# Kernel optimization log

Measured on AMD Instinct MI355X. Metric: run time of the kernel, lower is better.

Reference implementation:

```python
import jax, jax.numpy as jnp
import numpy as np

DIM = 512
HEADS = 16
DIM_HEAD = 64
INNER = HEADS * DIM_HEAD
MAX_T = 32
BASE = 10000.0


def rotate_half(t):
    t1, t2 = jnp.split(t, 2, axis=-1)
    return jnp.concatenate((-t2, t1), axis=-1)


def setup_inputs() -> dict:
    key = jax.random.key(0)
    ks = jax.random.split(key, 12)
    B, T, S = 2, 16, 128
    x = jax.random.normal(ks[0], (B, T, S, DIM), dtype=jnp.float32)
    y = jax.random.normal(ks[1], (B, T, S, DIM), dtype=jnp.float32)
    temporal_mask = jax.random.randint(ks[2], (B, T, T), 0, 2).astype(jnp.int32)
    sc = 1.0 / np.sqrt(DIM)
    Wq = jax.random.normal(ks[3], (DIM, INNER), dtype=jnp.float32) * sc
    Wk = jax.random.normal(ks[4], (DIM, INNER), dtype=jnp.float32) * sc
    Wv = jax.random.normal(ks[5], (DIM, INNER), dtype=jnp.float32) * sc
    Wo = jax.random.normal(ks[6], (INNER, DIM), dtype=jnp.float32) / np.sqrt(INNER)
    bo = jnp.zeros((DIM,), dtype=jnp.float32)
    pos_emb = jax.random.normal(ks[7], (MAX_T, DIM), dtype=jnp.float32)
    gate_w = jax.random.normal(ks[8], (DIM, 1), dtype=jnp.float32) * sc
    gate_b = jnp.zeros((1,), dtype=jnp.float32)
    return {"x": x, "y": y, "temporal_mask": temporal_mask, "Wq": Wq, "Wk": Wk,
            "Wv": Wv, "Wo": Wo, "bo": bo, "pos_emb": pos_emb,
            "gate_w": gate_w, "gate_b": gate_b}


def reference(x, y, temporal_mask, Wq, Wk, Wv, Wo, bo, pos_emb, gate_w, gate_b):
    B, T, S, D = x.shape
    n = T * S
    scale = DIM_HEAD ** (-0.5)
    # temporal positional embedding (T <= MAX_T path)
    tp = pos_emb[:T][None, :, None, :]  # [1,T,1,D]
    x = x + tp
    y = y + tp
    xf = x.reshape(B, n, D)
    yf = y.reshape(B, n, D)
    # NOTE: k is computed from x (as in the source), v from y
    q = (xf @ Wq).reshape(B, n, HEADS, DIM_HEAD).transpose(0, 2, 1, 3)
    k = (xf @ Wk).reshape(B, n, HEADS, DIM_HEAD).transpose(0, 2, 1, 3)
    v = (yf @ Wv).reshape(B, n, HEADS, DIM_HEAD).transpose(0, 2, 1, 3)
    # RoPE over flattened token index
    inv_freq = 1.0 / (BASE ** (jnp.arange(0, DIM_HEAD, 2, dtype=jnp.float32) / DIM_HEAD))
    freqs = jnp.arange(n, dtype=jnp.float32)[:, None] * inv_freq[None, :]  # [n, d/2]
    emb = jnp.concatenate((freqs, freqs), axis=-1)  # [n, d]
    fc = jnp.cos(emb)[None, None, :, :]
    fs = jnp.sin(emb)[None, None, :, :]
    q = q * fc + rotate_half(q) * fs
    k = k * fc + rotate_half(k) * fs
    dots = jnp.einsum('bhid,bhjd->bhij', q, k) * scale  # [B,H,n,n]
    # expand temporal mask [B,T,T] -> [B,1,n,n] block structure
    m = jnp.repeat(jnp.repeat(temporal_mask, S, axis=1), S, axis=2)[:, None, :, :]
    dots = jnp.where(m == 0, -jnp.inf, dots)
    attn = jax.nn.softmax(dots, axis=-1)
    out = jnp.einsum('bhij,bhjd->bhid', attn, v)  # [B,H,n,d]
    out = out.transpose(0, 2, 1, 3).reshape(B, n, INNER)
    out = out @ Wo + bo
    out = out.reshape(B, T, S, D)
    gate = jax.nn.sigmoid(out @ gate_w + gate_b)  # [B,T,S,1]
    return out * gate
```

## Files before the change

### kernel.cpp

```cpp
#include <hip/hip_runtime.h>
#include <hip/hip_bf16.h>

typedef __attribute__((ext_vector_type(4))) short short4v;
typedef __attribute__((ext_vector_type(8))) short short8v;
typedef __attribute__((ext_vector_type(4))) float float4v;
typedef __attribute__((ext_vector_type(2))) unsigned int uint2v;
typedef __attribute__((ext_vector_type(4))) unsigned int uint4v;

#define NTOK 2048
#define MROWS 4096
#define DMODEL 512
#define NINNER 1024
#define DH 64
#define HH 16
#define LOG2E 1.4426950408889634f

__device__ __forceinline__ unsigned short b2s(float f) {
    __hip_bfloat16 h = __float2bfloat16(f);
    return __builtin_bit_cast(unsigned short, h);
}
__device__ __forceinline__ float bf2f(unsigned short h) {
    unsigned int u = ((unsigned int)h) << 16;
    return __builtin_bit_cast(float, u);
}

__device__ __forceinline__ float4v mfma32(short8v a, short8v b, float4v c) {
    return __builtin_amdgcn_mfma_f32_16x16x32_bf16(a, b, c, 0, 0, 0);
}

__device__ __forceinline__ void gld16(const void* g, void* l) {
    __builtin_amdgcn_global_load_lds((const __attribute__((address_space(1))) void*)g,
                                     (__attribute__((address_space(3))) void*)l, 16, 0, 0);
}

__global__ void k_pre(const float* __restrict__ x, const float* __restrict__ y,
                      const float* __restrict__ pe,
                      unsigned short* __restrict__ xpb, unsigned short* __restrict__ ypb,
                      const float* __restrict__ Wq, const float* __restrict__ Wk,
                      const float* __restrict__ Wv, const float* __restrict__ Wo,
                      const float* __restrict__ gwv, const float* __restrict__ gbv,
                      const float* __restrict__ bo,
                      unsigned short* __restrict__ wall, unsigned short* __restrict__ wot,
                      float* __restrict__ ctab, float* __restrict__ stab,
                      unsigned short* __restrict__ gvp, float* __restrict__ bgp) {
    __shared__ float tl[64][65];
    const int blk = blockIdx.x;
    const int tid = threadIdx.x;
    if (blk < 2048) {
        int e0 = (blk * 256 + tid) * 4;
        int row = e0 >> 9, col = e0 & 511;
        int t = (row & (NTOK - 1)) >> 7;
        const float4v xv = *(const float4v*)(x + e0);
        const float4v yv = *(const float4v*)(y + e0);
        const float4v pv = *(const float4v*)(pe + t * DMODEL + col);
        short4v xo, yo;
#pragma unroll
        for (int i = 0; i < 4; ++i) {
            xo[i] = (short)b2s(xv[i] + pv[i]);
            yo[i] = (short)b2s(yv[i] + pv[i]);
        }
        *(short4v*)(xpb + e0) = xo;
        *(short4v*)(ypb + e0) = yo;
    } else if (blk < 2560) {
        int t = blk - 2048;
        const float* W;
        unsigned short* dst;
        int K, N, k0, n0;
        if (t < 384) {
            int which = t / 128, tile = t % 128;
            W = (which == 0) ? Wq : (which == 1) ? Wk : Wv;
            dst = wall + (size_t)which * 1024 * 512;
            K = 512; N = 1024;
            k0 = (tile >> 4) * 64; n0 = (tile & 15) * 64;
        } else {
            int tile = t - 384;
            W = Wo; dst = wot;
            K = 1024; N = 512;
            k0 = (tile >> 3) * 64; n0 = (tile & 7) * 64;
        }
        int tx = tid & 63, ty4 = tid >> 6;
#pragma unroll
        for (int p = 0; p < 16; ++p) {
            int ky = p * 4 + ty4;
            tl[ky][tx] = W[(size_t)(k0 + ky) * N + n0 + tx];
        }
        __syncthreads();
#pragma unroll
        for (int p = 0; p < 16; ++p) {
            int ny = p * 4 + ty4;
            dst[(size_t)(n0 + ny) * K + k0 + tx] = b2s(tl[tx][ny]);
        }
    } else if (blk < 2816) {
        int idx = (blk - 2560) * 256 + tid;
        int p = idx >> 5, j = idx & 31;
        float invf = powf(10000.0f, -(float)(2 * j) * (1.0f / 64.0f));
        float f = (float)p * invf;
        ctab[idx] = cosf(f);
        stab[idx] = sinf(f);
    } else if (blk < 2832) {
        int base = (blk - 2816) * 64;
        int w = tid >> 6, l = tid & 63, l16 = l & 15, g = l >> 4;
        int row = base + w * 16 + l16;
        const float* wr = Wo + (size_t)row * 512 + g * 128;
        const float* gr = gwv + g * 128;
        float s = 0.f;
#pragma unroll
        for (int t = 0; t < 32; ++t) {
            float4v a = *(const float4v*)(wr + t * 4);
            float4v b = *(const float4v*)(gr + t * 4);
            s += a[0] * b[0] + a[1] * b[1] + a[2] * b[2] + a[3] * b[3];
        }
        s += __shfl_xor(s, 16);
        s += __shfl_xor(s, 32);
        if (g == 0) gvp[row] = b2s(s);
    } else {
        if (tid < 64) {
            float s = 0.f;
#pragma unroll
            for (int t = 0; t < 8; ++t) s += bo[tid + t * 64] * gwv[tid + t * 64];
#pragma unroll
            for (int off = 32; off > 0; off >>= 1) s += __shfl_xor(s, off);
            if (tid == 0) bgp[0] = s + gbv[0];
        }
    }
}

__global__ __launch_bounds__(256) void k_qkv(const unsigned short* __restrict__ A,
                                             const unsigned short* __restrict__ A2,
                                             const unsigned short* __restrict__ Bt,
                                             unsigned short* __restrict__ Cq,
                                             unsigned short* __restrict__ Ck,
                                             unsigned short* __restrict__ Cvv,
                                             const float* __restrict__ ctab,
                                             const float* __restrict__ stab,
                                             float scale) {
    __shared__ unsigned short Ab[2][4096];
    __shared__ unsigned short Bb[2][4096];
    const int tid = threadIdx.x;
    const int w = tid >> 6, l = tid & 63, l16 = l & 15, g = l >> 4;
    const int wm = w >> 1, wn = w & 1;
    const int m0 = blockIdx.y * 128, n0 = blockIdx.x * 128;
    const unsigned short* Ap = (n0 >= 2048) ? A2 : A;
    float4v acc[4][4];
#pragma unroll
    for (int i = 0; i < 4; ++i)
#pragma unroll
        for (int j = 0; j < 4; ++j) acc[i][j] = (float4v){0.f, 0.f, 0.f, 0.f};

    auto stage = [&](int t, int buf) {
        int k0 = t * 32;
#pragma unroll
        for (int it = 0; it < 2; ++it) {
            int f = it * 4 + w;
            gld16(Ap + (size_t)(m0 + f * 16 + l16) * 512 + k0 + g * 8, &Ab[buf][f * 512]);
            gld16(Bt + (size_t)(n0 + f * 16 + l16) * 512 + k0 + g * 8, &Bb[buf][f * 512]);
        }
    };

    stage(0, 0);
    __syncthreads();
    for (int t = 0; t < 16; ++t) {
        const int cur = t & 1;
        if (t + 1 < 16) stage(t + 1, cur ^ 1);
        short8v af[4], bf[4];
#pragma unroll
        for (int mi = 0; mi < 4; ++mi)
            af[mi] = *(const short8v*)&Ab[cur][(wm * 4 + mi) * 512 + l * 8];
#pragma unroll
        for (int nj = 0; nj < 4; ++nj)
            bf[nj] = *(const short8v*)&Bb[cur][(wn * 4 + nj) * 512 + l * 8];
        __builtin_amdgcn_s_setprio(1);
#pragma unroll
        for (int mi = 0; mi < 4; ++mi)
#pragma unroll
            for (int nj = 0; nj < 4; ++nj)
                acc[mi][nj] = mfma32(af[mi], bf[nj], acc[mi][nj]);
        __builtin_amdgcn_s_setprio(0);
        __syncthreads();
    }

    const int hh = (n0 + wn * 64) >> 6;
    const int head = hh & 15;
    if (hh < 32) {
        unsigned short* out = (hh < 16) ? Cq : Ck;
        const float sc = (hh < 16) ? scale : 1.0f;
#pragma unroll
        for (int mi = 0; mi < 4; ++mi)
#pragma unroll
            for (int r = 0; r < 4; ++r) {
                int row = m0 + wm * 64 + mi * 16 + g * 4 + r;
                int b = row >> 11, pos = row & (NTOK - 1);
                const float* cr = ctab + pos * 32;
                const float* sr = stab + pos * 32;
                unsigned short* ob = out + (size_t)((b * HH + head) * NTOK + pos) * DH;
#pragma unroll
                for (int nj = 0; nj < 2; ++nj) {
                    int j = nj * 16 + l16;
                    float c = cr[j], s = sr[j];
                    float v1 = acc[mi][nj][r], v2 = acc[mi][nj + 2][r];
                    ob[j] = b2s((v1 * c - v2 * s) * sc);
                    ob[j + 32] = b2s((v2 * c + v1 * s) * sc);
                }
            }
    } else {
#pragma unroll
        for (int mi = 0; mi < 4; ++mi)
#pragma unroll
            for (int nj = 0; nj < 4; ++nj) {
                int d = nj * 16 + l16;
                int row0 = m0 + wm * 64 + mi * 16 + g * 4;
                int b = row0 >> 11, pos0 = row0 & (NTOK - 1);
                short4v o;
#pragma unroll
                for (int r = 0; r < 4; ++r) o[r] = (short)b2s(acc[mi][nj][r]);
                *(short4v*)(Cvv + (size_t)((b * HH + head) * DH + d) * NTOK + pos0) = o;
            }
    }
}

__global__ __launch_bounds__(256) void k_oproj(const unsigned short* __restrict__ A,
                                               const unsigned short* __restrict__ Bt,
                                               const float* __restrict__ bo,
                                               const unsigned short* __restrict__ gv,
                                               const float* __restrict__ bgp,
                                               float* __restrict__ out) {
    __shared__ unsigned short Ab[2][2048];
    __shared__ unsigned short Bb[2][2048];
    const int tid = threadIdx.x;
    const int w = tid >> 6, l = tid & 63, l16 = l & 15, g = l >> 4;
    const int m0 = blockIdx.y * 64, n0 = blockIdx.x * 64;
    float4v acc[4];
#pragma unroll
    for (int j = 0; j < 4; ++j) acc[j] = (float4v){0.f, 0.f, 0.f, 0.f};
    float4v gacc = (float4v){0.f, 0.f, 0.f, 0.f};

    auto stage = [&](int t, int buf) {
        int k0 = t * 32;
        gld16(A + (size_t)(m0 + w * 16 + l16) * 1024 + k0 + g * 8, &Ab[buf][w * 512]);
        gld16(Bt + (size_t)(n0 + w * 16 + l16) * 1024 + k0 + g * 8, &Bb[buf][w * 512]);
    };

    stage(0, 0);
    __syncthreads();
    for (int t = 0; t < 32; ++t) {
        const int cur = t & 1;
        if (t + 1 < 32) stage(t + 1, cur ^ 1);
        short8v af = *(const short8v*)&Ab[cur][w * 512 + l * 8];
        short8v bf[4];
#pragma unroll
        for (int nj = 0; nj < 4; ++nj)
            bf[nj] = *(const short8v*)&Bb[cur][nj * 512 + l * 8];
        short8v gvf = *(const short8v*)(gv + t * 32 + g * 8);
        __builtin_amdgcn_s_setprio(1);
#pragma unroll
        for (int nj = 0; nj < 4; ++nj)
            acc[nj] = mfma32(af, bf[nj], acc[nj]);
        gacc = mfma32(af, gvf, gacc);
        __builtin_amdgcn_s_setprio(0);
        __syncthreads();
    }
    const float bg = bgp[0];
    float gl[4];
#pragma unroll
    for (int r = 0; r < 4; ++r) gl[r] = 1.0f / (1.0f + __expf(-(gacc[r] + bg)));
#pragma unroll
    for (int nj = 0; nj < 4; ++nj) {
        int col = n0 + nj * 16 + l16;
        float bv = bo[col];
#pragma unroll
        for (int r = 0; r < 4; ++r) {
            int row = m0 + w * 16 + g * 4 + r;
            out[(size_t)row * 512 + col] = (acc[nj][r] + bv) * gl[r];
        }
    }
}

__global__ __launch_bounds__(512) void k_attn(const unsigned short* __restrict__ qh,
                                              const unsigned short* __restrict__ kh,
                                              const unsigned short* __restrict__ vt,
                                              const int* __restrict__ tmask,
                                              unsigned short* __restrict__ otmp) {
    __shared__ unsigned short Kb[3][4096];
    __shared__ unsigned short Vb[2][4096];
    __shared__ int tlist[33];
    const int blk = blockIdx.x;
    const int u = (blk & 7) * 64 + (blk >> 3);
    const int ti = u & 15, h = (u >> 4) & 15, b = u >> 8;
    const int tid = threadIdx.x, w = tid >> 6, l = tid & 63, l16 = l & 15, g = l >> 4;
    if (tid == 0) {
        int c = 0;
        for (int j = 0; j < 16; ++j)
            if (tmask[(b * 16 + ti) * 16 + j]) { tlist[c++] = 2 * j; tlist[c++] = 2 * j + 1; }
        tlist[32] = c;
    }
    __syncthreads();
    const int cnt = tlist[32];
    const unsigned short* qb = qh + (size_t)((b * HH + h) * NTOK) * DH;
    const unsigned short* kb = kh + (size_t)((b * HH + h) * NTOK) * DH;
    const unsigned short* vb = vt + (size_t)((b * HH + h) * DH) * NTOK;
    const int q0 = ti * 128 + w * 16;

    short8v qf[2];
#pragma unroll
    for (int c = 0; c < 2; ++c)
        qf[c] = *(const short8v*)(qb + (size_t)(q0 + l16) * DH + c * 32 + g * 8);

    short8v ones;
#pragma unroll
    for (int j = 0; j < 8; ++j) ones[j] = (short)0x3F80;

    float4v oacc[4];
#pragma unroll
    for (int i = 0; i < 4; ++i) oacc[i] = (float4v){0.f, 0.f, 0.f, 0.f};
    float4v lsum = (float4v){0.f, 0.f, 0.f, 0.f};
    float mx = -1e30f;
    uint4v vrg;
    float4v sA[4], sB[4];

    auto stageK = [&](int st, int buf) {
        const unsigned short* ga =
            kb + (size_t)(st * 64 + (w >> 1) * 16 + l16) * DH + (w & 1) * 32 + g * 8;
        gld16(ga, &Kb[buf][w * 512]);
    };
    auto loadV = [&](int st) {
        const unsigned short* ga =
            vb + (size_t)((w >> 1) * 16 + l16) * NTOK + st * 64 + (w & 1) * 32 + g * 4;
        uint2v lo = *(const uint2v*)ga;
        uint2v hi = *(const uint2v*)(ga + 16);
        vrg = (uint4v){lo[0], lo[1], hi[0], hi[1]};
    };
    auto writeV = [&](int buf) {
        *(uint4v*)&Vb[buf][w * 512 + l * 8] = vrg;
    };
    auto qkcomp = [&](int buf, float4v (&s)[4]) {
#pragma unroll
        for (int jk = 0; jk < 4; ++jk) s[jk] = (float4v){0.f, 0.f, 0.f, 0.f};
        __builtin_amdgcn_s_setprio(1);
#pragma unroll
        for (int jk = 0; jk < 4; ++jk) {
            short8v kf0 = *(const short8v*)&Kb[buf][(jk * 2 + 0) * 512 + l * 8];
            short8v kf1 = *(const short8v*)&Kb[buf][(jk * 2 + 1) * 512 + l * 8];
            s[jk] = mfma32(kf0, qf[0], s[jk]);
            s[jk] = mfma32(kf1, qf[1], s[jk]);
        }
        __builtin_amdgcn_s_setprio(0);
    };

    auto body = [&](int i, float4v (&scur)[4], float4v (&snext)[4]) {
        const bool pre1 = (i + 1 < cnt), pre2 = (i + 2 < cnt);
        if (pre2) stageK(tlist[i + 2], (i + 2) % 3);
        if (pre1) loadV(tlist[i + 1]);
        float tm = -1e30f;
#pragma unroll
        for (int jk = 0; jk < 4; ++jk) {
            float4v s4 = scur[jk];
            tm = fmaxf(tm, fmaxf(fmaxf(s4[0], s4[1]), fmaxf(s4[2], s4[3])));
        }
        tm = fmaxf(tm, __shfl_xor(tm, 16));
        tm = fmaxf(tm, __shfl_xor(tm, 32));
        if (!__all(tm <= mx + 8.0f)) {
            float mnew = fmaxf(mx, tm);
            float alpha = exp2f(mx - mnew);
#pragma unroll
            for (int r = 0; r < 4; ++r) lsum[r] *= alpha;
#pragma unroll
            for (int md = 0; md < 4; ++md)
#pragma unroll
                for (int r = 0; r < 4; ++r) oacc[md][r] *= alpha;
            mx = mnew;
        }
        if (pre1) qkcomp((i + 1) % 3, snext);
        short8v pf[2];
#pragma unroll
        for (int cc = 0; cc < 2; ++cc) {
            short8v pv;
#pragma unroll
            for (int r = 0; r < 4; ++r) {
                pv[r] = (short)b2s(exp2f(scur[2 * cc][r] - mx));
                pv[r + 4] = (short)b2s(exp2f(scur[2 * cc + 1][r] - mx));
            }
            pf[cc] = pv;
        }
        __builtin_amdgcn_s_setprio(1);
#pragma unroll
        for (int cc = 0; cc < 2; ++cc) lsum = mfma32(ones, pf[cc], lsum);
#pragma unroll
        for (int md = 0; md < 4; ++md)
#pragma unroll
            for (int cc = 0; cc < 2; ++cc) {
                short8v vf = *(const short8v*)&Vb[i & 1][(md * 2 + cc) * 512 + l * 8];
                oacc[md] = mfma32(vf, pf[cc], oacc[md]);
            }
        __builtin_amdgcn_s_setprio(0);
        if (pre1) writeV((i + 1) & 1);
        __syncthreads();
    };

    if (cnt > 0) {
        stageK(tlist[0], 0);
        loadV(tlist[0]);
        if (cnt > 1) stageK(tlist[1], 1);
        writeV(0);
        __syncthreads();
        qkcomp(0, sA);
        for (int i = 0; i < cnt; i += 2) {
            body(i, sA, sB);
            if (i + 1 < cnt) body(i + 1, sB, sA);
        }
    }
    float lrow = lsum[0];
    float inv = lrow > 0.f ? 1.0f / lrow : 0.f;
    int q = q0 + l16;
#pragma unroll
    for (int md = 0; md < 4; ++md) {
        short4v o;
#pragma unroll
        for (int r = 0; r < 4; ++r) o[r] = (short)b2s(oacc[md][r] * inv);
        *(short4v*)(otmp + (size_t)(b * NTOK + q) * NINNER + h * DH + md * 16 + g * 4) = o;
    }
}

extern "C" void kernel_launch(void* const* d_in, const int* in_sizes, int n_in,
                              void* d_out, int out_size, void* d_ws, size_t ws_size,
                              hipStream_t stream) {
    (void)in_sizes; (void)n_in; (void)out_size; (void)ws_size;
    const float* x = (const float*)d_in[0];
    const float* y = (const float*)d_in[1];
    const int* tmask = (const int*)d_in[2];
    const float* Wq = (const float*)d_in[3];
    const float* Wk = (const float*)d_in[4];
    const float* Wv = (const float*)d_in[5];
    const float* Wo = (const float*)d_in[6];
    const float* bo = (const float*)d_in[7];
    const float* pe = (const float*)d_in[8];
    const float* gw = (const float*)d_in[9];
    const float* gb = (const float*)d_in[10];

    char* ws = (char*)d_ws;
    const size_t MB = 1u << 20;
    unsigned short* xpb  = (unsigned short*)(ws + 0);
    unsigned short* ypb  = (unsigned short*)(ws + 4 * MB);
    unsigned short* wall = (unsigned short*)(ws + 8 * MB);
    unsigned short* wot  = (unsigned short*)(ws + 11 * MB);
    unsigned short* qh   = (unsigned short*)(ws + 12 * MB);
    unsigned short* kh   = (unsigned short*)(ws + 20 * MB);
    unsigned short* vt   = (unsigned short*)(ws + 28 * MB);
    unsigned short* otm  = (unsigned short*)(ws + 36 * MB);
    float* ct = (float*)(ws + 44 * MB);
    float* st = (float*)(ws + 44 * MB + 256 * 1024);
    unsigned short* gv = (unsigned short*)(ws + 45 * MB);
    float* bg = (float*)(ws + 45 * MB + 4096);
    float* outp = (float*)d_out;

    k_pre<<<2833, 256, 0, stream>>>(x, y, pe, xpb, ypb, Wq, Wk, Wv, Wo, gw, gb, bo,
                                    wall, wot, ct, st, gv, bg);
    k_qkv<<<dim3(24, 32), 256, 0, stream>>>(xpb, ypb, wall, qh, kh, vt, ct, st,
                                            0.125f * LOG2E);
    k_attn<<<512, 512, 0, stream>>>(qh, kh, vt, tmask, otm);
    k_oproj<<<dim3(8, 64), 256, 0, stream>>>(otm, wot, bo, gv, bg, outp);
}
```

Before: 115.6 us.

## Process two key tiles per iteration with four-deep K/V LDS ring buffers

Restructures the attention inner loop to handle two 64-key tiles per iteration. Both QK products, a shared max/rescale and both PV products run together, and K and V for the next pair are prefetched into a four-slot LDS ring. This halves the number of block-wide barriers and online-softmax rescale checks and gives more independent MFMA work to schedule. In exchange it uses more LDS (four K and four V buffers) and more registers, which may lower occupancy. It also removes the previous overlap of the next tile's QK with the current tile's softmax.

```diff
diff --git a/kernel.cpp b/kernel.cpp
--- a/kernel.cpp
+++ b/kernel.cpp
@@ -280,8 +280,8 @@
                                               const unsigned short* __restrict__ vt,
                                               const int* __restrict__ tmask,
                                               unsigned short* __restrict__ otmp) {
-    __shared__ unsigned short Kb[3][4096];
-    __shared__ unsigned short Vb[2][4096];
+    __shared__ unsigned short Kb[4][4096];
+    __shared__ unsigned short Vb[4][4096];
     __shared__ int tlist[33];
     const int blk = blockIdx.x;
     const int u = (blk & 7) * 64 + (blk >> 3);
@@ -314,7 +314,7 @@
     for (int i = 0; i < 4; ++i) oacc[i] = (float4v){0.f, 0.f, 0.f, 0.f};
     float4v lsum = (float4v){0.f, 0.f, 0.f, 0.f};
     float mx = -1e30f;
-    uint4v vrg;
+    uint4v vrgA, vrgB;
     float4v sA[4], sB[4];
 
     auto stageK = [&](int st, int buf) {
@@ -322,15 +322,15 @@
             kb + (size_t)(st * 64 + (w >> 1) * 16 + l16) * DH + (w & 1) * 32 + g * 8;
         gld16(ga, &Kb[buf][w * 512]);
     };
-    auto loadV = [&](int st) {
+    auto loadV = [&](int st, uint4v& vr) {
         const unsigned short* ga =
             vb + (size_t)((w >> 1) * 16 + l16) * NTOK + st * 64 + (w & 1) * 32 + g * 4;
         uint2v lo = *(const uint2v*)ga;
         uint2v hi = *(const uint2v*)(ga + 16);
-        vrg = (uint4v){lo[0], lo[1], hi[0], hi[1]};
-    };
-    auto writeV = [&](int buf) {
-        *(uint4v*)&Vb[buf][w * 512 + l * 8] = vrg;
+        vr = (uint4v){lo[0], lo[1], hi[0], hi[1]};
+    };
+    auto writeV = [&](int buf, const uint4v& vr) {
+        *(uint4v*)&Vb[buf][w * 512 + l * 8] = vr;
     };
     auto qkcomp = [&](int buf, float4v (&s)[4]) {
 #pragma unroll
@@ -345,19 +345,30 @@
         }
         __builtin_amdgcn_s_setprio(0);
     };
-
-    auto body = [&](int i, float4v (&scur)[4], float4v (&snext)[4]) {
-        const bool pre1 = (i + 1 < cnt), pre2 = (i + 2 < cnt);
-        if (pre2) stageK(tlist[i + 2], (i + 2) % 3);
-        if (pre1) loadV(tlist[i + 1]);
-        float tm = -1e30f;
-#pragma unroll
-        for (int jk = 0; jk < 4; ++jk) {
-            float4v s4 = scur[jk];
-            tm = fmaxf(tm, fmaxf(fmaxf(s4[0], s4[1]), fmaxf(s4[2], s4[3])));
-        }
-        tm = fmaxf(tm, __shfl_xor(tm, 16));
-        tm = fmaxf(tm, __shfl_xor(tm, 32));
+    auto packexp = [&](const float4v (&s)[4], short8v (&pf)[2]) {
+#pragma unroll
+        for (int cc = 0; cc < 2; ++cc) {
+            short8v pv;
+#pragma unroll
+            for (int r = 0; r < 4; ++r) {
+                pv[r] = (short)b2s(exp2f(s[2 * cc][r] - mx));
+                pv[r + 4] = (short)b2s(exp2f(s[2 * cc + 1][r] - mx));
+            }
+            pf[cc] = pv;
+        }
+    };
+    auto pvcomp = [&](int buf, const short8v (&pf)[2]) {
+#pragma unroll
+        for (int cc = 0; cc < 2; ++cc) lsum = mfma32(ones, pf[cc], lsum);
+#pragma unroll
+        for (int md = 0; md < 4; ++md)
+#pragma unroll
+            for (int cc = 0; cc < 2; ++cc) {
+                short8v vf = *(const short8v*)&Vb[buf][(md * 2 + cc) * 512 + l * 8];
+                oacc[md] = mfma32(vf, pf[cc], oacc[md]);
+            }
+    };
+    auto rescale = [&](float tm) {
         if (!__all(tm <= mx + 8.0f)) {
             float mnew = fmaxf(mx, tm);
             float alpha = exp2f(mx - mnew);
@@ -369,43 +380,58 @@
                 for (int r = 0; r < 4; ++r) oacc[md][r] *= alpha;
             mx = mnew;
         }
-        if (pre1) qkcomp((i + 1) % 3, snext);
-        short8v pf[2];
-#pragma unroll
-        for (int cc = 0; cc < 2; ++cc) {
-            short8v pv;
-#pragma unroll
-            for (int r = 0; r < 4; ++r) {
-                pv[r] = (short)b2s(exp2f(scur[2 * cc][r] - mx));
-                pv[r + 4] = (short)b2s(exp2f(scur[2 * cc + 1][r] - mx));
-            }
-            pf[cc] = pv;
-        }
-        __builtin_amdgcn_s_setprio(1);
-#pragma unroll
-        for (int cc = 0; cc < 2; ++cc) lsum = mfma32(ones, pf[cc], lsum);
-#pragma unroll
-        for (int md = 0; md < 4; ++md)
-#pragma unroll
-            for (int cc = 0; cc < 2; ++cc) {
-                short8v vf = *(const short8v*)&Vb[i & 1][(md * 2 + cc) * 512 + l * 8];
-                oacc[md] = mfma32(vf, pf[cc], oacc[md]);
-            }
-        __builtin_amdgcn_s_setprio(0);
-        if (pre1) writeV((i + 1) & 1);
-        __syncthreads();
     };
 
     if (cnt > 0) {
         stageK(tlist[0], 0);
-        loadV(tlist[0]);
-        if (cnt > 1) stageK(tlist[1], 1);
-        writeV(0);
+        loadV(tlist[0], vrgA);
+        if (cnt > 1) { stageK(tlist[1], 1); loadV(tlist[1], vrgB); }
+        writeV(0, vrgA);
+        if (cnt > 1) writeV(1, vrgB);
         __syncthreads();
-        qkcomp(0, sA);
-        for (int i = 0; i < cnt; i += 2) {
-            body(i, sA, sB);
-            if (i + 1 < cnt) body(i + 1, sB, sA);
+        int i = 0;
+        while (i + 1 < cnt) {
+            const bool pre2 = (i + 2 < cnt), pre3 = (i + 3 < cnt);
+            if (pre2) { stageK(tlist[i + 2], (i + 2) & 3); loadV(tlist[i + 2], vrgA); }
+            if (pre3) { stageK(tlist[i + 3], (i + 3) & 3); loadV(tlist[i + 3], vrgB); }
+            qkcomp(i & 3, sA);
+            qkcomp((i + 1) & 3, sB);
+            float tm = -1e30f;
+#pragma unroll
+            for (int jk = 0; jk < 4; ++jk) {
+                float4v a4 = sA[jk], b4 = sB[jk];
+                tm = fmaxf(tm, fmaxf(fmaxf(a4[0], a4[1]), fmaxf(a4[2], a4[3])));
+                tm = fmaxf(tm, fmaxf(fmaxf(b4[0], b4[1]), fmaxf(b4[2], b4[3])));
+            }
+            tm = fmaxf(tm, __shfl_xor(tm, 16));
+            tm = fmaxf(tm, __shfl_xor(tm, 32));
+            rescale(tm);
+            short8v pfA[2], pfB[2];
+            packexp(sA, pfA);
+            packexp(sB, pfB);
+            __builtin_amdgcn_s_setprio(1);
+            pvcomp(i & 3, pfA);
+            pvcomp((i + 1) & 3, pfB);
+            __builtin_amdgcn_s_setprio(0);
+            if (pre2) writeV((i + 2) & 3, vrgA);
+            if (pre3) writeV((i + 3) & 3, vrgB);
+            __syncthreads();
+            i += 2;
+        }
+        if (i < cnt) {
+            qkcomp(i & 3, sA);
+            float tm = -1e30f;
+#pragma unroll
+            for (int jk = 0; jk < 4; ++jk) {
+                float4v a4 = sA[jk];
+                tm = fmaxf(tm, fmaxf(fmaxf(a4[0], a4[1]), fmaxf(a4[2], a4[3])));
+            }
+            tm = fmaxf(tm, __shfl_xor(tm, 16));
+            tm = fmaxf(tm, __shfl_xor(tm, 32));
+            rescale(tm);
+            short8v pfA[2];
+            packexp(sA, pfA);
+            pvcomp(i & 3, pfA);
         }
     }
     float lrow = lsum[0];
```

Result: slower. 122.6 us (+6.1%).

## Schedule attention blocks by mask-derived work count for load balance

Applied to the files above, without the earlier changes.

Adds eight blocks to the preprocessing kernel that count the active temporal keys for each attention work unit, sort the units by that count, and write a block schedule interleaving heavy and light units. The attention kernel then reads its work unit from this schedule instead of a fixed mapping. The goal is to even out per-CU load, since the masked tiles make work per block very uneven. The cost is a serial insertion sort in one thread per group and an extra global read per attention block.

```diff
diff --git a/kernel.cpp b/kernel.cpp
--- a/kernel.cpp
+++ b/kernel.cpp
@@ -39,11 +39,13 @@
                       const float* __restrict__ Wq, const float* __restrict__ Wk,
                       const float* __restrict__ Wv, const float* __restrict__ Wo,
                       const float* __restrict__ gwv, const float* __restrict__ gbv,
-                      const float* __restrict__ bo,
+                      const float* __restrict__ bo, const int* __restrict__ tmask,
                       unsigned short* __restrict__ wall, unsigned short* __restrict__ wot,
                       float* __restrict__ ctab, float* __restrict__ stab,
-                      unsigned short* __restrict__ gvp, float* __restrict__ bgp) {
+                      unsigned short* __restrict__ gvp, float* __restrict__ bgp,
+                      int* __restrict__ schd) {
     __shared__ float tl[64][65];
+    __shared__ int scnt[64];
     const int blk = blockIdx.x;
     const int tid = threadIdx.x;
     if (blk < 2048) {
@@ -113,7 +115,7 @@
         s += __shfl_xor(s, 16);
         s += __shfl_xor(s, 32);
         if (g == 0) gvp[row] = b2s(s);
-    } else {
+    } else if (blk == 2832) {
         if (tid < 64) {
             float s = 0.f;
 #pragma unroll
@@ -121,6 +123,31 @@
 #pragma unroll
             for (int off = 32; off > 0; off >>= 1) s += __shfl_xor(s, off);
             if (tid == 0) bgp[0] = s + gbv[0];
+        }
+    } else {
+        int kx = blk - 2833;
+        if (tid < 64) {
+            int uu = kx * 64 + tid;
+            int tti = uu & 15, bb = uu >> 8;
+            int m = 0;
+#pragma unroll
+            for (int jj = 0; jj < 16; ++jj)
+                m += (tmask[(bb * 16 + tti) * 16 + jj] != 0);
+            scnt[tid] = m;
+        }
+        __syncthreads();
+        if (tid == 0) {
+            int cnt[64], idx[64];
+            for (int j = 0; j < 64; ++j) { cnt[j] = scnt[j]; idx[j] = j; }
+            for (int a = 1; a < 64; ++a) {
+                int c = cnt[a], id = idx[a], p = a - 1;
+                while (p >= 0 && cnt[p] < c) { cnt[p+1] = cnt[p]; idx[p+1] = idx[p]; --p; }
+                cnt[p+1] = c; idx[p+1] = id;
+            }
+            for (int j = 0; j < 32; ++j) {
+                schd[8 * j + kx] = kx * 64 + idx[j];
+                schd[8 * (j + 32) + kx] = kx * 64 + idx[63 - j];
+            }
         }
     }
 }
@@ -279,12 +306,13 @@
                                               const unsigned short* __restrict__ kh,
                                               const unsigned short* __restrict__ vt,
                                               const int* __restrict__ tmask,
+                                              const int* __restrict__ schd,
                                               unsigned short* __restrict__ otmp) {
     __shared__ unsigned short Kb[3][4096];
     __shared__ unsigned short Vb[2][4096];
     __shared__ int tlist[33];
     const int blk = blockIdx.x;
-    const int u = (blk & 7) * 64 + (blk >> 3);
+    const int u = schd[blk];
     const int ti = u & 15, h = (u >> 4) & 15, b = u >> 8;
     const int tid = threadIdx.x, w = tid >> 6, l = tid & 63, l16 = l & 15, g = l >> 4;
     if (tid == 0) {
@@ -450,12 +478,13 @@
     float* st = (float*)(ws + 44 * MB + 256 * 1024);
     unsigned short* gv = (unsigned short*)(ws + 45 * MB);
     float* bg = (float*)(ws + 45 * MB + 4096);
+    int* schd = (int*)(ws + 45 * MB + 8192);
     float* outp = (float*)d_out;
 
-    k_pre<<<2833, 256, 0, stream>>>(x, y, pe, xpb, ypb, Wq, Wk, Wv, Wo, gw, gb, bo,
-                                    wall, wot, ct, st, gv, bg);
+    k_pre<<<2841, 256, 0, stream>>>(x, y, pe, xpb, ypb, Wq, Wk, Wv, Wo, gw, gb, bo,
+                                    tmask, wall, wot, ct, st, gv, bg, schd);
     k_qkv<<<dim3(24, 32), 256, 0, stream>>>(xpb, ypb, wall, qh, kh, vt, ct, st,
                                             0.125f * LOG2E);
-    k_attn<<<512, 512, 0, stream>>>(qh, kh, vt, tmask, otm);
+    k_attn<<<512, 512, 0, stream>>>(qh, kh, vt, tmask, schd, otm);
     k_oproj<<<dim3(8, 64), 256, 0, stream>>>(otm, wot, bo, gv, bg, outp);
 }
```

After: 261.2 us. 126% more time.
